# Kernel tuning notes

Measured on AMD Instinct MI355X. Metric: run time of the kernel, lower is better.

Reference implementation:

```python
import jax, jax.numpy as jnp
import numpy as np

NUM_ENTITIES = 100000
BATCH_SIZE = 4096
E_STATIC = 250000
E_NEW = 4096
D_ENT = 128
D_REL = 64
N_REL = 9
N_TYPES = 3
N_INTENTS = 8
NUM_LAYERS = 3
SCALE = 0.05


def _make_edges(key, n):
    ks = jax.random.split(key, 5)
    src = jax.random.randint(ks[0], (n,), 0, NUM_ENTITIES, dtype=jnp.int32)
    st = jax.random.randint(ks[1], (n,), 0, N_TYPES, dtype=jnp.int32)
    tgt = jax.random.randint(ks[2], (n,), 0, NUM_ENTITIES, dtype=jnp.int32)
    tt = jax.random.randint(ks[3], (n,), 0, N_TYPES, dtype=jnp.int32)
    rel = jax.random.randint(ks[4], (n,), 0, N_REL, dtype=jnp.int32)
    return jnp.stack([src, st, tgt, tt, rel], axis=1)


def setup_inputs() -> dict:
    key = jax.random.key(0)
    ks = jax.random.split(key, 16)
    return {
        'new_edges': _make_edges(ks[0], E_NEW),
        'new_node_types': jax.random.randint(ks[1], (BATCH_SIZE,), 0, N_TYPES, dtype=jnp.int32),
        'static_edges': _make_edges(ks[2], E_STATIC),
        'entity_embeddings': SCALE * jax.random.normal(ks[3], (NUM_ENTITIES - BATCH_SIZE, D_ENT), jnp.float32),
        'default_emb': SCALE * jax.random.normal(ks[4], (N_TYPES, D_ENT), jnp.float32),
        'relation_emb': SCALE * jax.random.normal(ks[5], (N_REL, D_REL), jnp.float32),
        'W_rel': SCALE * jax.random.normal(ks[6], (N_REL, D_ENT, D_REL), jnp.float32),
        'b_rel': SCALE * jax.random.normal(ks[7], (N_REL, D_REL), jnp.float32),
        'W_msg': SCALE * jax.random.normal(ks[8], (N_REL, D_ENT, D_ENT), jnp.float32),
        'W_intent': SCALE * jax.random.normal(ks[9], (N_TYPES, D_ENT, N_INTENTS), jnp.float32),
        'b_intent': SCALE * jax.random.normal(ks[10], (N_TYPES, N_INTENTS), jnp.float32),
        'W_ibn': SCALE * jax.random.normal(ks[11], (N_TYPES, N_INTENTS, N_REL), jnp.float32),
        'b_ibn': SCALE * jax.random.normal(ks[12], (N_TYPES, N_REL), jnp.float32),
    }


def multi_dense(lookups, values, W, b=None, act=None):
    # Same math as tf.gather(W, lookups) followed by values @ w, but computed
    # against all D (<=9) weight slices then selected, to avoid materializing
    # a [E, d_in, d_out] gathered-weights tensor.
    out_all = jnp.einsum('ei,dio->edo', values, W)  # [E, D, d_out]
    out = jnp.take_along_axis(out_all, lookups[:, None, None], axis=1)[:, 0]
    if b is not None:
        out = out + b[lookups]
    return act(out) if act is not None else out


def reference(new_edges, new_node_types, static_edges, entity_embeddings,
              default_emb, relation_emb, W_rel, b_rel, W_msg,
              W_intent, b_intent, W_ibn, b_ibn):
    edges = jnp.concatenate([new_edges, static_edges], axis=0)  # [E, 5]
    sources = edges[:, 0]
    targets = edges[:, 2]
    target_types = edges[:, 3]
    relations = edges[:, 4]

    rel_e = relation_emb[relations]  # [E, D_REL]
    # first BATCH_SIZE entity slots come from type default embeddings
    ent = jnp.concatenate([default_emb[new_node_types], entity_embeddings], axis=0)  # [N, D_ENT]

    layer_edge_weights = []
    for _ in range(NUM_LAYERS):
        src = ent[sources]  # [E, D_ENT]
        tgt = ent[targets]  # [E, D_ENT]
        # per-target intent distribution and per-relation intent weights
        intents = multi_dense(target_types, tgt, W_intent, b_intent, jax.nn.softmax)  # [E, N_INTENTS]
        rel_w = multi_dense(target_types, intents, W_ibn, b_ibn, jax.nn.softmax)  # [E, N_REL]
        iw = jnp.take_along_axis(rel_w, relations[:, None], axis=1)[:, 0]  # [E]
        # per-relation transform of source embeddings
        src_rel = multi_dense(relations, src, W_rel, b_rel, jax.nn.selu)  # [E, D_REL]
        scores = jnp.einsum('er,er,e->e', src_rel, rel_e, iw)  # [E]
        exp_s = jnp.exp(scores)
        denom = jax.ops.segment_sum(exp_s, targets, num_segments=NUM_ENTITIES)  # [N]
        # tf.math.reciprocal_no_nan semantics
        safe = jnp.where(denom != 0, denom, 1.0)
        recip = jnp.where(denom != 0, 1.0 / safe, 0.0)
        dist = exp_s * recip[targets]  # scatter-softmax over incoming edges
        # inference: dropout is identity
        msg = dist[:, None] * multi_dense(relations, src, W_msg, None, None)  # [E, D_ENT]
        ent = jax.ops.segment_sum(msg, targets, num_segments=NUM_ENTITIES)  # [N, D_ENT]
        layer_edge_weights.append(dist)

    return ent, jnp.stack(layer_edge_weights)  # [N, D_ENT], [L, E]
```

## Files before the change

### kernel.cpp

```cpp
#include <hip/hip_runtime.h>
#include <cstddef>
#include <cstdint>

#define NE 100000
#define EN 4096
#define ET 254096
#define D 128
#define DR 64
#define NR 9
#define NT 3
#define NI 8
#define TE 256
#define TILES_X 28

using frag  = __attribute__((ext_vector_type(8))) short;
using f32x4 = __attribute__((ext_vector_type(4))) float;

__device__ __forceinline__ ushort f2b(float x) {
  union { float f; uint32_t u; } v; v.f = x;
  uint32_t r = v.u + 0x7FFFu + ((v.u >> 16) & 1u);
  return (ushort)(r >> 16);
}

__device__ __forceinline__ uint32_t cvtpk(float lo, float hi) {
  uint32_t r;
  asm("v_cvt_pk_bf16_f32 %0, %1, %2" : "=v"(r) : "v"(lo), "v"(hi));
  return r;
}

__device__ __forceinline__ frag lds_rd(const ushort* b, int row, int k) {
  const int ch = ((k >> 3) ^ (row & 7));
  return *(const frag*)(b + row * D + (ch << 3));
}
__device__ __forceinline__ void lds_wr(ushort* b, int row, int ch, frag v) {
  *(frag*)(b + row * D + ((ch ^ (row & 7)) << 3)) = v;
}
__device__ __forceinline__ void lds_wr2(ushort* b, int row, int k, uint32_t v) {
  const int ch = (k >> 3) ^ (row & 7);
  *(uint32_t*)(b + row * D + (ch << 3) + (k & 7)) = v;
}

__global__ void k_init(ushort* __restrict__ entb, const int* __restrict__ ntypes,
                       const float* __restrict__ def, const float* __restrict__ emb) {
  int i = blockIdx.x * blockDim.x + threadIdx.x;
  if (i >= NE * (D / 4)) return;
  int row = i >> 5, ch = i & 31;
  float4 v;
  if (row < EN) v = ((const float4*)(def + ntypes[row] * D))[ch];
  else v = ((const float4*)(emb + (size_t)(row - EN) * D))[ch];
  ushort4 h;
  h.x = f2b(v.x); h.y = f2b(v.y); h.z = f2b(v.z); h.w = f2b(v.w);
  ((ushort4*)entb)[i] = h;
}

__global__ void k_zero_cnt(int* cnt) { if (threadIdx.x < 48) cnt[threadIdx.x] = 0; }

__global__ __launch_bounds__(256) void k_wconv(const float* __restrict__ Wr,
                                               const float* __restrict__ Wm,
                                               ushort* __restrict__ wrelb,
                                               ushort* __restrict__ wmsgb) {
  const int nrel = NR * DR * (D / 8);
  const int nmsg = NR * D * (D / 8);
  int idx = blockIdx.x * 256 + threadIdx.x;
  if (idx < nrel) {
    int r = idx / (DR * 16), rem = idx % (DR * 16), n = rem / 16, sc = rem % 16;
    int kb = (sc ^ (n & 7)) * 8;
    const float* s = Wr + (size_t)r * D * DR + (size_t)kb * DR + n;
    uint4 pk;
    pk.x = cvtpk(s[0 * DR], s[1 * DR]); pk.y = cvtpk(s[2 * DR], s[3 * DR]);
    pk.z = cvtpk(s[4 * DR], s[5 * DR]); pk.w = cvtpk(s[6 * DR], s[7 * DR]);
    *(uint4*)(wrelb + (size_t)r * DR * D + n * D + sc * 8) = pk;
  } else if (idx < nrel + nmsg) {
    int j = idx - nrel;
    int r = j / (D * 16), rem = j % (D * 16), n = rem / 16, sc = rem % 16;
    int kb = (sc ^ (n & 7)) * 8;
    const float* s = Wm + (size_t)r * D * D + (size_t)kb * D + n;
    uint4 pk;
    pk.x = cvtpk(s[0 * D], s[1 * D]); pk.y = cvtpk(s[2 * D], s[3 * D]);
    pk.z = cvtpk(s[4 * D], s[5 * D]); pk.w = cvtpk(s[6 * D], s[7 * D]);
    *(uint4*)(wmsgb + (size_t)r * D * D + n * D + sc * 8) = pk;
  }
}

__global__ __launch_bounds__(256) void k_hist2(const int* __restrict__ nedg,
                                               const int* __restrict__ sedg,
                                               int* __restrict__ cnt,
                                               int* __restrict__ thist) {
  __shared__ int h[NR];
  if (threadIdx.x < NR) h[threadIdx.x] = 0;
  __syncthreads();
  int e = blockIdx.x * 256 + threadIdx.x;
  if (e < ET) {
    const int* p = (e < EN) ? nedg + (size_t)e * 5 : sedg + (size_t)(e - EN) * 5;
    atomicAdd(&h[p[4]], 1);
    atomicAdd(&thist[p[2]], 1);
  }
  __syncthreads();
  if (threadIdx.x < NR && h[threadIdx.x]) atomicAdd(&cnt[threadIdx.x], h[threadIdx.x]);
}

__global__ void k_prefix(const int* __restrict__ cnt, int* __restrict__ base,
                         int* __restrict__ head) {
  if (threadIdx.x == 0) {
    int acc = 0;
    for (int r = 0; r < NR; r++) { base[r] = acc; head[r] = acc; acc += cnt[r]; }
  }
}

__global__ __launch_bounds__(256) void k_scan1(const int* __restrict__ hist,
                                               int* __restrict__ local_ex,
                                               int* __restrict__ bsum, int n) {
  __shared__ int s[256];
  int i = blockIdx.x * 256 + threadIdx.x;
  int v = (i < n) ? hist[i] : 0;
  s[threadIdx.x] = v;
  __syncthreads();
  for (int off = 1; off < 256; off <<= 1) {
    int t = (threadIdx.x >= off) ? s[threadIdx.x - off] : 0;
    __syncthreads();
    s[threadIdx.x] += t;
    __syncthreads();
  }
  if (i < n) local_ex[i] = s[threadIdx.x] - v;
  if (threadIdx.x == 255) bsum[blockIdx.x] = s[255];
}

__global__ __launch_bounds__(512) void k_scan2(int* __restrict__ bsum, int nb) {
  __shared__ int s[512];
  int v = (threadIdx.x < nb) ? bsum[threadIdx.x] : 0;
  s[threadIdx.x] = v;
  __syncthreads();
  for (int off = 1; off < 512; off <<= 1) {
    int t = (threadIdx.x >= off) ? s[threadIdx.x - off] : 0;
    __syncthreads();
    s[threadIdx.x] += t;
    __syncthreads();
  }
  if (threadIdx.x < nb) bsum[threadIdx.x] = s[threadIdx.x] - v;
}

__global__ void k_scan3(int* __restrict__ tgt_off, const int* __restrict__ bsum,
                        int* __restrict__ thead) {
  int i = blockIdx.x * 256 + threadIdx.x;
  if (i < NE) {
    int v = tgt_off[i] + bsum[i >> 8];
    tgt_off[i] = v;
    thead[i] = v;
  }
  if (i == 0) tgt_off[NE] = ET;
}

__global__ __launch_bounds__(256) void k_scatter3(const int* __restrict__ nedg,
                                                  const int* __restrict__ sedg,
                                                  int* __restrict__ head,
                                                  int* __restrict__ thead,
                                                  int4* __restrict__ epack,
                                                  int* __restrict__ esorted) {
  __shared__ int h[NR], bb[NR];
  if (threadIdx.x < NR) h[threadIdx.x] = 0;
  __syncthreads();
  int e = blockIdx.x * 256 + threadIdx.x;
  int r = -1, pos = 0, s = 0, t = 0, tt = 0;
  if (e < ET) {
    const int* p = (e < EN) ? nedg + (size_t)e * 5 : sedg + (size_t)(e - EN) * 5;
    s = p[0]; t = p[2]; tt = p[3]; r = p[4];
    pos = atomicAdd(&h[r], 1);
  }
  __syncthreads();
  if (threadIdx.x < NR)
    bb[threadIdx.x] = h[threadIdx.x] ? atomicAdd(&head[threadIdx.x], h[threadIdx.x]) : 0;
  __syncthreads();
  if (r >= 0) {
    int pt = atomicAdd(&thead[t], 1);
    epack[bb[r] + pos] = make_int4(s, (t * NT + tt) * NR, pt, 0);
    esorted[pt] = e;
  }
}

__global__ __launch_bounds__(1024) void k_iw(
    const ushort* __restrict__ entb,
    const float* __restrict__ W_int, const float* __restrict__ b_int,
    const float* __restrict__ W_ibn, const float* __restrict__ b_ibn,
    float* __restrict__ IW) {
  __shared__ ushort sE[256 * D];
  __shared__ ushort sWi[NT * 16 * D];
  __shared__ float sInt3[256 * 25];
  __shared__ float sbint[NT * NI], sWibn[NT * NI * NR], sbibn[NT * NR];

  const int tid = threadIdx.x;
  const int lane = tid & 63, wv = tid >> 6, g = lane >> 4, c = lane & 15;

  {
    float a[2], b[2];
#pragma unroll
    for (int j = 0; j < 2; j++) {
      int i = tid + j * 1024;
      if (i < NT * NI * (D / 2)) {
        int tt = i / (NI * D / 2), rem = i % (NI * D / 2), jj = rem / (D / 2), k2 = rem % (D / 2);
        const float* Wi = W_int + (size_t)tt * D * NI;
        a[j] = Wi[(2 * k2) * NI + jj]; b[j] = Wi[(2 * k2 + 1) * NI + jj];
      }
    }
#pragma unroll
    for (int j = 0; j < 2; j++) {
      int i = tid + j * 1024;
      if (i < NT * NI * (D / 2)) {
        int tt = i / (NI * D / 2), rem = i % (NI * D / 2), jj = rem / (D / 2), k2 = rem % (D / 2);
        lds_wr2(sWi, tt * 16 + jj, 2 * k2, cvtpk(a[j], b[j]));
      }
    }
  }
  for (int i = tid; i < NT * 8 * (D / 2); i += 1024) {
    int tt = i / (8 * D / 2), rem = i % (8 * D / 2), j = rem / (D / 2), k2 = rem % (D / 2);
    lds_wr2(sWi, tt * 16 + 8 + j, 2 * k2, 0u);
  }
  if (tid < NT * NI) sbint[tid] = b_int[tid];
  for (int i = tid; i < NT * NI * NR; i += 1024) sWibn[i] = W_ibn[i];
  if (tid < NT * NR) sbibn[tid] = b_ibn[tid];

  const int ebase = blockIdx.x * 256;
  const int nrow = min(256, NE - ebase);
  {
    frag tmp[4];
#pragma unroll
    for (int j = 0; j < 4; j++) {
      int i = tid + j * 1024, row = i >> 4, ch = i & 15;
      tmp[j] = (row < nrow) ? ((const frag*)(entb + (size_t)(ebase + row) * D))[ch] : (frag){};
    }
#pragma unroll
    for (int j = 0; j < 4; j++) {
      int i = tid + j * 1024, row = i >> 4, ch = i & 15;
      lds_wr(sE, row, ch, tmp[j]);
    }
  }
  __syncthreads();

  {
    f32x4 accI[NT];
#pragma unroll
    for (int tt = 0; tt < NT; tt++) accI[tt] = (f32x4){0.f, 0.f, 0.f, 0.f};
#pragma unroll
    for (int ks = 0; ks < 4; ks++) {
      const int k = ks * 32 + g * 8;
      frag a = lds_rd(sE, wv * 16 + c, k);
#pragma unroll
      for (int tt = 0; tt < NT; tt++) {
        frag b = lds_rd(sWi, tt * 16 + c, k);
        accI[tt] = __builtin_amdgcn_mfma_f32_16x16x32_bf16(a, b, accI[tt], 0, 0, 0);
      }
    }
    if (c < NI) {
      const int rb = wv * 16 + g * 4;
#pragma unroll
      for (int tt = 0; tt < NT; tt++)
#pragma unroll
        for (int q = 0; q < 4; q++) sInt3[(rb + q) * 25 + tt * 8 + c] = accI[tt][q];
    }
  }
  __syncthreads();

  float* stg = (float*)sE;
  {
    const int row = tid & 255, tt = tid >> 8;
    if (tt < NT && row < nrow) {
      float it[NI], mx = -1e30f;
#pragma unroll
      for (int j = 0; j < NI; j++) {
        it[j] = sInt3[row * 25 + tt * 8 + j] + sbint[tt * NI + j];
        mx = fmaxf(mx, it[j]);
      }
      float ssum = 0.f;
#pragma unroll
      for (int j = 0; j < NI; j++) { it[j] = __expf(it[j] - mx); ssum += it[j]; }
      const float inv = 1.f / ssum;
      float qv[NR];
#pragma unroll
      for (int k = 0; k < NR; k++) qv[k] = sbibn[tt * NR + k];
#pragma unroll
      for (int j = 0; j < NI; j++) {
        const float ij = it[j] * inv;
#pragma unroll
        for (int k = 0; k < NR; k++) qv[k] = fmaf(ij, sWibn[(tt * NI + j) * NR + k], qv[k]);
      }
      float m9 = qv[0];
#pragma unroll
      for (int k = 1; k < NR; k++) m9 = fmaxf(m9, qv[k]);
      float s9 = 0.f;
#pragma unroll
      for (int k = 0; k < NR; k++) s9 += __expf(qv[k] - m9);
      const float i9 = 1.f / s9;
#pragma unroll
      for (int k = 0; k < NR; k++) stg[row * 27 + tt * 9 + k] = __expf(qv[k] - m9) * i9;
    }
  }
  __syncthreads();

  const int n27 = nrow * 27;
  float* outp = IW + (size_t)ebase * 27;
  for (int i = tid; i < n27; i += 1024) outp[i] = stg[i];
}

__global__ __launch_bounds__(1024) void k_pass1(
    const ushort* __restrict__ entb,
    const int4* __restrict__ epack,
    const int* __restrict__ cnt, const int* __restrict__ base_g,
    const float* __restrict__ IW,
    const float* __restrict__ rel_emb, const float* __restrict__ b_rel,
    const ushort* __restrict__ wrelb, const ushort* __restrict__ wmsgb,
    ushort* __restrict__ msgbuf, float* __restrict__ exps_s) {
  const int r = blockIdx.y;
  __shared__ ushort sA[TE * D];
  __shared__ ushort sWm[D * D];
  __shared__ ushort sWr[DR * D];
  __shared__ int sTP[TE];
  __shared__ float sIW[TE];
  __shared__ float sbrel[DR], srele[DR];

  const int tid = threadIdx.x;
  const int lane = tid & 63;
  const int wv = tid >> 6;
  const int g = lane >> 4;
  const int c = lane & 15;
  const int row = tid & 255, h = tid >> 8;

  {
    const frag* wr = (const frag*)(wrelb + (size_t)r * DR * D);
    ((frag*)sWr)[tid] = wr[tid];
    const frag* wm = (const frag*)(wmsgb + (size_t)r * D * D);
    ((frag*)sWm)[tid] = wm[tid];
    ((frag*)sWm)[tid + 1024] = wm[tid + 1024];
  }
  if (tid < DR) { sbrel[tid] = b_rel[r * DR + tid]; srele[tid] = rel_emb[r * DR + tid]; }

  const int nr = cnt[r];
  const int bbase = base_g[r];
  const int ntiles = (nr + TE - 1) / TE;

  int4 mp; frag tmp[4]; float iwv = 0.f;
  auto prefetch = [&](int t_) {
    int eidx = t_ * TE + row;
    if (eidx >= nr) eidx = 0;
    mp = epack[bbase + eidx];
    const frag* rp = (const frag*)(entb + (size_t)mp.x * D);
#pragma unroll
    for (int j = 0; j < 4; j++) tmp[j] = rp[h * 4 + j];
    iwv = IW[mp.y + r];
  };

  int tile = blockIdx.x;
  if (tile < ntiles) prefetch(tile);

  for (; tile < ntiles; tile += gridDim.x) {
    const int ne = min(TE, nr - tile * TE);
    __syncthreads();

#pragma unroll
    for (int j = 0; j < 4; j++) lds_wr(sA, row, h * 4 + j, tmp[j]);
    if (h == 0) { sTP[row] = mp.z; sIW[row] = iwv; }
    __syncthreads();

    const int nxt = tile + gridDim.x;
    if (nxt < ntiles) prefetch(nxt);

    f32x4 accR[4], accM[8];
#pragma unroll
    for (int nt = 0; nt < 4; nt++) accR[nt] = (f32x4){0.f, 0.f, 0.f, 0.f};
#pragma unroll
    for (int nt = 0; nt < 8; nt++) accM[nt] = (f32x4){0.f, 0.f, 0.f, 0.f};
#pragma unroll
    for (int ks = 0; ks < 4; ks++) {
      const int k = ks * 32 + g * 8;
      frag a0 = lds_rd(sA, wv * 16 + c, k);
#pragma unroll
      for (int nt = 0; nt < 4; nt++) {
        frag b = lds_rd(sWr, nt * 16 + c, k);
        accR[nt] = __builtin_amdgcn_mfma_f32_16x16x32_bf16(a0, b, accR[nt], 0, 0, 0);
      }
#pragma unroll
      for (int nt = 0; nt < 8; nt++) {
        frag b = lds_rd(sWm, nt * 16 + c, k);
        accM[nt] = __builtin_amdgcn_mfma_f32_16x16x32_bf16(a0, b, accM[nt], 0, 0, 0);
      }
    }

    const int mb = wv * 16 + g * 4;

    float es[4];
    {
      float v[4] = {0.f, 0.f, 0.f, 0.f};
#pragma unroll
      for (int nt = 0; nt < 4; nt++) {
        const int col = nt * 16 + c;
        const float br = sbrel[col], re = srele[col];
#pragma unroll
        for (int q = 0; q < 4; q++) {
          const float x = accR[nt][q] + br;
          const float sl = x > 0.f ? 1.0507009873554805f * x
                                   : 1.7580993408473766f * (__expf(x) - 1.f);
          v[q] = fmaf(sl, re, v[q]);
        }
      }
#pragma unroll
      for (int off = 1; off < 16; off <<= 1)
#pragma unroll
        for (int q = 0; q < 4; q++) v[q] += __shfl_xor(v[q], off, 64);
#pragma unroll
      for (int q = 0; q < 4; q++) {
        const int m = mb + q;
        es[q] = __expf(v[q] * sIW[m]);
        if (c == 0 && m < ne) exps_s[sTP[m]] = es[q];
      }
    }

    {
#pragma unroll
      for (int q = 0; q < 4; q++) {
        const int m = mb + q;
        ushort* mrow = msgbuf + (size_t)sTP[m] * D;
#pragma unroll
        for (int nt = 0; nt < 8; nt++) {
          float val = accM[nt][q] * es[q];
          float other = __shfl_xor(val, 1, 64);
          if (!(c & 1) && m < ne)
            *(uint32_t*)(mrow + nt * 16 + c) = cvtpk(val, other);
        }
      }
    }
  }
}

__global__ __launch_bounds__(256) void k_agg(
    const ushort* __restrict__ msgbuf, const float* __restrict__ exps_s,
    const int* __restrict__ tgt_off, const int* __restrict__ esorted,
    ushort* __restrict__ entb, float* __restrict__ fout,
    float* __restrict__ dout, int last) {
  const int lg = threadIdx.x & 15;
  const int grp = threadIdx.x >> 4;
  const int ngrp = gridDim.x * 16;
  for (int t = blockIdx.x * 16 + grp; t < NE; t += ngrp) {
    const int beg = tgt_off[t], end = tgt_off[t + 1];
    float a[8] = {0.f, 0.f, 0.f, 0.f, 0.f, 0.f, 0.f, 0.f};
    float dsum = 0.f;
    for (int j = beg; j < end; j++) {
      const uint4 pk = *(const uint4*)(msgbuf + (size_t)j * D + lg * 8);
      dsum += exps_s[j];
      a[0] += __uint_as_float(pk.x << 16); a[1] += __uint_as_float(pk.x & 0xFFFF0000u);
      a[2] += __uint_as_float(pk.y << 16); a[3] += __uint_as_float(pk.y & 0xFFFF0000u);
      a[4] += __uint_as_float(pk.z << 16); a[5] += __uint_as_float(pk.z & 0xFFFF0000u);
      a[6] += __uint_as_float(pk.w << 16); a[7] += __uint_as_float(pk.w & 0xFFFF0000u);
    }
    const float rec = (dsum != 0.f) ? 1.f / dsum : 0.f;
#pragma unroll
    for (int i = 0; i < 8; i++) a[i] *= rec;
    if (last) {
      float4* o = (float4*)(fout + (size_t)t * D + lg * 8);
      o[0] = make_float4(a[0], a[1], a[2], a[3]);
      o[1] = make_float4(a[4], a[5], a[6], a[7]);
    } else {
      uint4 pk;
      pk.x = (uint32_t)f2b(a[0]) | ((uint32_t)f2b(a[1]) << 16);
      pk.y = (uint32_t)f2b(a[2]) | ((uint32_t)f2b(a[3]) << 16);
      pk.z = (uint32_t)f2b(a[4]) | ((uint32_t)f2b(a[5]) << 16);
      pk.w = (uint32_t)f2b(a[6]) | ((uint32_t)f2b(a[7]) << 16);
      *(uint4*)(entb + (size_t)t * D + lg * 8) = pk;
    }
    for (int j = beg + lg; j < end; j += 16) dout[esorted[j]] = exps_s[j] * rec;
  }
}

extern "C" void kernel_launch(void* const* d_in, const int* in_sizes, int n_in,
                              void* d_out, int out_size, void* d_ws, size_t ws_size,
                              hipStream_t stream) {
  const int* nedg = (const int*)d_in[0];
  const int* ntypes = (const int*)d_in[1];
  const int* sedg = (const int*)d_in[2];
  const float* emb = (const float*)d_in[3];
  const float* def = (const float*)d_in[4];
  const float* rel_emb = (const float*)d_in[5];
  const float* W_rel = (const float*)d_in[6];
  const float* b_rel = (const float*)d_in[7];
  const float* W_msg = (const float*)d_in[8];
  const float* W_int = (const float*)d_in[9];
  const float* b_int = (const float*)d_in[10];
  const float* W_ibn = (const float*)d_in[11];
  const float* b_ibn = (const float*)d_in[12];
  float* out = (float*)d_out;

  char* w = (char*)d_ws;
  size_t off = 0;
  ushort* entb = (ushort*)(w + off); off += (size_t)NE * D * 2;
  ushort* msgbuf = (ushort*)(w + off); off += (size_t)ET * D * 2;
  float* exps_s = (float*)(w + off); off += (size_t)ET * 4;
  int4* epack = (int4*)(w + off); off += (size_t)ET * 16;
  int* esorted = (int*)(w + off); off += (size_t)ET * 4;
  int* tgt_off = (int*)(w + off); off += (size_t)(NE + 4) * 4;
  int* thead = (int*)(w + off); off += (size_t)NE * 4;
  int* thist = (int*)(w + off); off += (size_t)NE * 4;
  int* bsum = (int*)(w + off); off += 2048;
  int* cnt = (int*)(w + off); off += 192;
  float* IW = (float*)(w + off); off += (size_t)NE * NT * NR * 4;
  ushort* wrelb = (ushort*)(w + off); off += (size_t)NR * DR * D * 2;
  ushort* wmsgb = (ushort*)(w + off); off += (size_t)NR * D * D * 2;
  int* base_g = cnt + 16;
  int* head = cnt + 32;
  float* dist_base = out + (size_t)NE * D;

  const int eblocks = (ET + 255) / 256;
  const int nb = (NE + 255) / 256;
  const int wblocks = (NR * DR * (D / 8) + NR * D * (D / 8) + 255) / 256;

  k_init<<<dim3((NE * (D / 4) + 255) / 256), 256, 0, stream>>>(entb, ntypes, def, emb);
  k_zero_cnt<<<1, 64, 0, stream>>>(cnt);
  hipMemsetAsync(thist, 0, (size_t)NE * 4, stream);
  k_wconv<<<dim3(wblocks), 256, 0, stream>>>(W_rel, W_msg, wrelb, wmsgb);
  k_hist2<<<dim3(eblocks), 256, 0, stream>>>(nedg, sedg, cnt, thist);
  k_prefix<<<1, 64, 0, stream>>>(cnt, base_g, head);
  k_scan1<<<dim3(nb), 256, 0, stream>>>(thist, tgt_off, bsum, NE);
  k_scan2<<<1, 512, 0, stream>>>(bsum, nb);
  k_scan3<<<dim3(nb), 256, 0, stream>>>(tgt_off, bsum, thead);
  k_scatter3<<<dim3(eblocks), 256, 0, stream>>>(nedg, sedg, head, thead, epack, esorted);

  for (int l = 0; l < 3; l++) {
    k_iw<<<dim3(nb), 1024, 0, stream>>>(entb, W_int, b_int, W_ibn, b_ibn, IW);
    k_pass1<<<dim3(TILES_X, NR), 1024, 0, stream>>>(
        entb, epack, cnt, base_g, IW, rel_emb, b_rel, wrelb, wmsgb, msgbuf, exps_s);
    k_agg<<<dim3(2048), 256, 0, stream>>>(msgbuf, exps_s, tgt_off, esorted, entb, out,
                                          dist_base + (size_t)l * ET, l == 2);
  }
}
```

Before: 340.1 us.

## Move dist output scatter to separate coalesced kernel and add nontemporal hints

```diff
diff --git a/kernel.cpp b/kernel.cpp
--- a/kernel.cpp
+++ b/kernel.cpp
@@ -15,6 +15,7 @@
 
 using frag  = __attribute__((ext_vector_type(8))) short;
 using f32x4 = __attribute__((ext_vector_type(4))) float;
+using u32x4 = __attribute__((ext_vector_type(4))) unsigned int;
 
 __device__ __forceinline__ ushort f2b(float x) {
   union { float f; uint32_t u; } v; v.f = x;
@@ -155,7 +156,7 @@
                                                   int* __restrict__ head,
                                                   int* __restrict__ thead,
                                                   int4* __restrict__ epack,
-                                                  int* __restrict__ esorted) {
+                                                  int2* __restrict__ tp2) {
   __shared__ int h[NR], bb[NR];
   if (threadIdx.x < NR) h[threadIdx.x] = 0;
   __syncthreads();
@@ -173,7 +174,7 @@
   if (r >= 0) {
     int pt = atomicAdd(&thead[t], 1);
     epack[bb[r] + pos] = make_int4(s, (t * NT + tt) * NR, pt, 0);
-    esorted[pt] = e;
+    tp2[e] = make_int2(pt, t);
   }
 }
 
@@ -408,7 +409,7 @@
       for (int q = 0; q < 4; q++) {
         const int m = mb + q;
         es[q] = __expf(v[q] * sIW[m]);
-        if (c == 0 && m < ne) exps_s[sTP[m]] = es[q];
+        if (c == 0 && m < ne) __builtin_nontemporal_store(es[q], &exps_s[sTP[m]]);
       }
     }
 
@@ -422,7 +423,7 @@
           float val = accM[nt][q] * es[q];
           float other = __shfl_xor(val, 1, 64);
           if (!(c & 1) && m < ne)
-            *(uint32_t*)(mrow + nt * 16 + c) = cvtpk(val, other);
+            __builtin_nontemporal_store(cvtpk(val, other), (uint32_t*)(mrow + nt * 16 + c));
         }
       }
     }
@@ -431,9 +432,9 @@
 
 __global__ __launch_bounds__(256) void k_agg(
     const ushort* __restrict__ msgbuf, const float* __restrict__ exps_s,
-    const int* __restrict__ tgt_off, const int* __restrict__ esorted,
+    const int* __restrict__ tgt_off,
     ushort* __restrict__ entb, float* __restrict__ fout,
-    float* __restrict__ dout, int last) {
+    float* __restrict__ drec, int last) {
   const int lg = threadIdx.x & 15;
   const int grp = threadIdx.x >> 4;
   const int ngrp = gridDim.x * 16;
@@ -442,7 +443,7 @@
     float a[8] = {0.f, 0.f, 0.f, 0.f, 0.f, 0.f, 0.f, 0.f};
     float dsum = 0.f;
     for (int j = beg; j < end; j++) {
-      const uint4 pk = *(const uint4*)(msgbuf + (size_t)j * D + lg * 8);
+      const u32x4 pk = __builtin_nontemporal_load((const u32x4*)(msgbuf + (size_t)j * D + lg * 8));
       dsum += exps_s[j];
       a[0] += __uint_as_float(pk.x << 16); a[1] += __uint_as_float(pk.x & 0xFFFF0000u);
       a[2] += __uint_as_float(pk.y << 16); a[3] += __uint_as_float(pk.y & 0xFFFF0000u);
@@ -450,6 +451,7 @@
       a[6] += __uint_as_float(pk.w << 16); a[7] += __uint_as_float(pk.w & 0xFFFF0000u);
     }
     const float rec = (dsum != 0.f) ? 1.f / dsum : 0.f;
+    if (lg == 0) drec[t] = rec;
 #pragma unroll
     for (int i = 0; i < 8; i++) a[i] *= rec;
     if (last) {
@@ -464,8 +466,17 @@
       pk.w = (uint32_t)f2b(a[6]) | ((uint32_t)f2b(a[7]) << 16);
       *(uint4*)(entb + (size_t)t * D + lg * 8) = pk;
     }
-    for (int j = beg + lg; j < end; j += 16) dout[esorted[j]] = exps_s[j] * rec;
-  }
+  }
+}
+
+__global__ __launch_bounds__(256) void k_dist2(const int2* __restrict__ tp2,
+                                               const float* __restrict__ exps_s,
+                                               const float* __restrict__ drec,
+                                               float* __restrict__ dout) {
+  int e = blockIdx.x * 256 + threadIdx.x;
+  if (e >= ET) return;
+  const int2 v = tp2[e];
+  dout[e] = exps_s[v.x] * drec[v.y];
 }
 
 extern "C" void kernel_launch(void* const* d_in, const int* in_sizes, int n_in,
@@ -492,10 +503,11 @@
   ushort* msgbuf = (ushort*)(w + off); off += (size_t)ET * D * 2;
   float* exps_s = (float*)(w + off); off += (size_t)ET * 4;
   int4* epack = (int4*)(w + off); off += (size_t)ET * 16;
-  int* esorted = (int*)(w + off); off += (size_t)ET * 4;
+  int2* tp2 = (int2*)(w + off); off += (size_t)ET * 8;
   int* tgt_off = (int*)(w + off); off += (size_t)(NE + 4) * 4;
   int* thead = (int*)(w + off); off += (size_t)NE * 4;
   int* thist = (int*)(w + off); off += (size_t)NE * 4;
+  float* drec = (float*)(w + off); off += (size_t)NE * 4;
   int* bsum = (int*)(w + off); off += 2048;
   int* cnt = (int*)(w + off); off += 192;
   float* IW = (float*)(w + off); off += (size_t)NE * NT * NR * 4;
@@ -511,20 +523,21 @@
 
   k_init<<<dim3((NE * (D / 4) + 255) / 256), 256, 0, stream>>>(entb, ntypes, def, emb);
   k_zero_cnt<<<1, 64, 0, stream>>>(cnt);
-  hipMemsetAsync(thist, 0, (size_t)NE * 4, stream);
+  (void)hipMemsetAsync(thist, 0, (size_t)NE * 4, stream);
   k_wconv<<<dim3(wblocks), 256, 0, stream>>>(W_rel, W_msg, wrelb, wmsgb);
   k_hist2<<<dim3(eblocks), 256, 0, stream>>>(nedg, sedg, cnt, thist);
   k_prefix<<<1, 64, 0, stream>>>(cnt, base_g, head);
   k_scan1<<<dim3(nb), 256, 0, stream>>>(thist, tgt_off, bsum, NE);
   k_scan2<<<1, 512, 0, stream>>>(bsum, nb);
   k_scan3<<<dim3(nb), 256, 0, stream>>>(tgt_off, bsum, thead);
-  k_scatter3<<<dim3(eblocks), 256, 0, stream>>>(nedg, sedg, head, thead, epack, esorted);
+  k_scatter3<<<dim3(eblocks), 256, 0, stream>>>(nedg, sedg, head, thead, epack, tp2);
 
   for (int l = 0; l < 3; l++) {
     k_iw<<<dim3(nb), 1024, 0, stream>>>(entb, W_int, b_int, W_ibn, b_ibn, IW);
     k_pass1<<<dim3(TILES_X, NR), 1024, 0, stream>>>(
         entb, epack, cnt, base_g, IW, rel_emb, b_rel, wrelb, wmsgb, msgbuf, exps_s);
-    k_agg<<<dim3(2048), 256, 0, stream>>>(msgbuf, exps_s, tgt_off, esorted, entb, out,
-                                          dist_base + (size_t)l * ET, l == 2);
-  }
-}
+    k_agg<<<dim3(2048), 256, 0, stream>>>(msgbuf, exps_s, tgt_off, entb, out, drec, l == 2);
+    k_dist2<<<dim3(eblocks), 256, 0, stream>>>(tp2, exps_s, drec,
+                                               dist_base + (size_t)l * ET);
+  }
+}
```

New measurement: 417.5 us. 1.23x slower.
